# Optimization experiments

Measured on AMD Instinct MI355X. Metric: run time of the kernel, lower is better.

## Reference

```python
import jax, jax.numpy as jnp
import numpy as np

LN_EPS = 1e-5
L2_EPS = 1e-12
SCALE = 1.0 / np.sqrt(768.0)
TOPK = 8


def _ln(x, g, b):
    m = jnp.mean(x, axis=-1, keepdims=True)
    v = jnp.mean(jnp.square(x - m), axis=-1, keepdims=True)
    return (x - m) * jax.lax.rsqrt(v + LN_EPS) * g + b


def _l2norm(x):
    n = jnp.sqrt(jnp.sum(jnp.square(x), axis=-1, keepdims=True))
    return x / jnp.maximum(n, L2_EPS)


def _topk_normalize(scores, k):
    # scores: [B, K]; keep top-k, zero rest, renormalize to sum 1
    vals, idx = jax.lax.top_k(scores, k)
    B = scores.shape[0]
    weights = jnp.zeros_like(scores).at[jnp.arange(B)[:, None], idx].set(vals)
    denom = jnp.maximum(jnp.sum(weights, axis=1, keepdims=True), 1e-8)
    return weights / denom


def setup_inputs() -> dict:
    key = jax.random.key(0)
    ks = jax.random.split(key, 8)
    B, N, D, K, H, C = 32, 4096, 768, 64, 3072, 1000
    inp = {
        "patch_tokens": jax.random.normal(ks[0], (B, N, D), jnp.float32),
        "global_features": jax.random.normal(ks[1], (B, D), jnp.float32),
        "base_logits": jax.random.normal(ks[2], (B, C), jnp.float32),
        "bq": jax.random.normal(ks[3], (K, D), jnp.float32) * 0.02,
        "qn_g": jnp.ones((D,)), "qn_b": jnp.zeros((D,)),
        "tn_g": jnp.ones((D,)), "tn_b": jnp.zeros((D,)),
        "bn_g": jnp.ones((D,)), "bn_b": jnp.zeros((D,)),
        "gn_g": jnp.ones((D,)), "gn_b": jnp.zeros((D,)),
        "rln_g": jnp.ones((D,)), "rln_b": jnp.zeros((D,)),
        "rw1": jax.random.normal(ks[4], (D, H), jnp.float32) / np.sqrt(D),
        "rb1": jnp.zeros((H,)),
        "rw2": jax.random.normal(ks[5], (H, 1), jnp.float32) / np.sqrt(H),
        "rb2": jnp.zeros((1,)),
        "hw1": jax.random.normal(ks[6], (2 * D, H), jnp.float32) / np.sqrt(2 * D),
        "hb1": jnp.zeros((H,)),
        "hw2": jax.random.normal(ks[7], (H, C), jnp.float32) / np.sqrt(H),
        "hb2": jnp.zeros((C,)),
    }
    return inp


def reference(patch_tokens, global_features, base_logits, bq,
              qn_g, qn_b, tn_g, tn_b, bn_g, bn_b, gn_g, gn_b,
              rln_g, rln_b, rw1, rb1, rw2, rb2, hw1, hb1, hw2, hb2):
    # normalized cross-attention: K basis queries vs N tokens
    tokens_key = _l2norm(_ln(patch_tokens, tn_g, tn_b))           # [B,N,D]
    queries = _l2norm(_ln(bq, qn_g, qn_b))                        # [K,D]
    attn_logits = jnp.einsum('kd,bnd->bkn', queries, tokens_key) * SCALE
    attn_weights = jax.nn.softmax(attn_logits, axis=-1)           # [B,K,N]
    basis_states = jnp.einsum('bkn,bnd->bkd', attn_weights, patch_tokens)
    # routing head: LN -> Linear -> GELU -> Linear -> softplus
    r = _ln(basis_states, rln_g, rln_b)
    r = jax.nn.gelu(r @ rw1 + rb1, approximate=False)
    routing_scores = jax.nn.softplus((r @ rw2 + rb2)[..., 0])     # [B,K]
    routing_weights = _topk_normalize(routing_scores, TOPK)
    basis_summary = jnp.einsum('bk,bkd->bd', routing_weights, basis_states)
    basis_summary = _ln(basis_summary, bn_g, bn_b)
    global_summary = _ln(global_features, gn_g, gn_b)
    fused = jnp.concatenate([global_summary, basis_summary], axis=-1)
    h = jax.nn.gelu(fused @ hw1 + hb1, approximate=False)
    residual_logits = h @ hw2 + hb2
    final_logits = base_logits + residual_logits
    # diversity loss over basis queries
    bqn = _l2norm(bq)
    gram = bqn @ bqn.T
    diversity_loss = jnp.mean(jnp.square(gram - jnp.eye(gram.shape[0], dtype=gram.dtype)))
    sparse_loss = jnp.mean(routing_scores)
    return (final_logits, residual_logits, routing_weights, sparse_loss, diversity_loss)
```

## Files before the change

kernel.cpp:

```cpp
#include <hip/hip_runtime.h>
#include <math.h>

#define SCALE 0.036084391824351613f

typedef unsigned short us;
typedef __attribute__((ext_vector_type(8))) short short8;
typedef __attribute__((ext_vector_type(4))) short short4s;
typedef __attribute__((ext_vector_type(4))) float f32x4;
#define MFMA16(a, b, c) __builtin_amdgcn_mfma_f32_16x16x32_bf16(a, b, c, 0, 0, 0)

__device__ __forceinline__ us f2bf(float f) {
  unsigned u = __float_as_uint(f);
  unsigned r = (u + 0x7fffu + ((u >> 16) & 1u)) >> 16;
  return (us)r;
}
__device__ __forceinline__ float bf2f(us u) { return __uint_as_float(((unsigned)u) << 16); }

__device__ __forceinline__ void split8(f32x4 a, f32x4 b, short8& hi, short8& lo) {
  float x[8] = {a[0], a[1], a[2], a[3], b[0], b[1], b[2], b[3]};
#pragma unroll
  for (int i = 0; i < 8; i++) {
    us h = f2bf(x[i]);
    hi[i] = (short)h;
    lo[i] = (short)f2bf(x[i] - bf2f(h));
  }
}

__device__ __forceinline__ float blockReduceSum(float v, float* sh) {
#pragma unroll
  for (int o = 32; o > 0; o >>= 1) v += __shfl_xor(v, o, 64);
  int lane = threadIdx.x & 63, wid = threadIdx.x >> 6;
  __syncthreads();
  if (lane == 0) sh[wid] = v;
  __syncthreads();
  float r = sh[0];
  int nw = blockDim.x >> 6;
  for (int i = 1; i < nw; i++) r += sh[i];
  return r;
}

__device__ __forceinline__ float blockReduceMax(float v, float* sh) {
#pragma unroll
  for (int o = 32; o > 0; o >>= 1) v = fmaxf(v, __shfl_xor(v, o, 64));
  int lane = threadIdx.x & 63, wid = threadIdx.x >> 6;
  __syncthreads();
  if (lane == 0) sh[wid] = v;
  __syncthreads();
  float r = sh[0];
  int nw = blockDim.x >> 6;
  for (int i = 1; i < nw; i++) r = fmaxf(r, sh[i]);
  return r;
}

__device__ __forceinline__ float gelu_exact(float x) {
  return 0.5f * x * (1.0f + erff(x * 0.7071067811865476f));
}

__global__ void __launch_bounds__(256) k_prep_queries(
    const float* __restrict__ bq, const float* __restrict__ qn_g, const float* __restrict__ qn_b,
    const float* __restrict__ tn_g, const float* __restrict__ tn_b,
    us* __restrict__ qgh, us* __restrict__ qgl,
    float* __restrict__ s1, float* __restrict__ qb,
    float* __restrict__ bqn, float* __restrict__ gcons) {
  __shared__ float sh[8];
  int k = blockIdx.x, t = threadIdx.x;
  const float* xr = bq + (size_t)k * 768;
  float x0 = xr[t], x1 = xr[t + 256], x2 = xr[t + 512];
  float sx = blockReduceSum(x0 + x1 + x2, sh);
  float sxx = blockReduceSum(x0 * x0 + x1 * x1 + x2 * x2, sh);
  float mean = sx * (1.0f / 768.0f);
  float var = fmaxf(sxx * (1.0f / 768.0f) - mean * mean, 0.0f);
  float rs = rsqrtf(var + 1e-5f);
  float y0 = (x0 - mean) * rs * qn_g[t] + qn_b[t];
  float y1 = (x1 - mean) * rs * qn_g[t + 256] + qn_b[t + 256];
  float y2 = (x2 - mean) * rs * qn_g[t + 512] + qn_b[t + 512];
  float ss = blockReduceSum(y0 * y0 + y1 * y1 + y2 * y2, sh);
  float inv = 1.0f / fmaxf(sqrtf(ss), 1e-12f);
  float q0 = y0 * inv, q1 = y1 * inv, q2 = y2 * inv;
  float tg0 = tn_g[t], tg1 = tn_g[t + 256], tg2 = tn_g[t + 512];
  float tb0 = tn_b[t], tb1 = tn_b[t + 256], tb2 = tn_b[t + 512];
  float g0 = q0 * tg0, g1 = q1 * tg1, g2 = q2 * tg2;
  us h0 = f2bf(g0), h1 = f2bf(g1), h2 = f2bf(g2);
  qgh[(size_t)k * 768 + t] = h0;
  qgh[(size_t)k * 768 + t + 256] = h1;
  qgh[(size_t)k * 768 + t + 512] = h2;
  qgl[(size_t)k * 768 + t] = f2bf(g0 - bf2f(h0));
  qgl[(size_t)k * 768 + t + 256] = f2bf(g1 - bf2f(h1));
  qgl[(size_t)k * 768 + t + 512] = f2bf(g2 - bf2f(h2));
  float s1p = blockReduceSum(g0 + g1 + g2, sh);
  float qbp = blockReduceSum(q0 * tb0 + q1 * tb1 + q2 * tb2, sh);
  if (t == 0) { s1[k] = s1p; qb[k] = qbp; }
  float inv2 = 1.0f / fmaxf(sqrtf(sxx), 1e-12f);
  bqn[(size_t)k * 768 + t] = x0 * inv2;
  bqn[(size_t)k * 768 + t + 256] = x1 * inv2;
  bqn[(size_t)k * 768 + t + 512] = x2 * inv2;
  float sggp = blockReduceSum(tg0 * tg0 + tg1 * tg1 + tg2 * tg2, sh);
  float sgbp = blockReduceSum(tg0 * tb0 + tg1 * tb1 + tg2 * tb2, sh);
  float sbbp = blockReduceSum(tb0 * tb0 + tb1 * tb1 + tb2 * tb2, sh);
  if (k == 0 && t == 0) { gcons[0] = sggp; gcons[1] = sgbp; gcons[2] = sbbp; }
}

__global__ void __launch_bounds__(256) k_gram(const float* __restrict__ bqn,
                                              float* __restrict__ gpart) {
  __shared__ float bk[768];
  __shared__ float arr[64];
  int k = blockIdx.x, t = threadIdx.x;
  bk[t] = bqn[(size_t)k * 768 + t];
  bk[t + 256] = bqn[(size_t)k * 768 + t + 256];
  bk[t + 512] = bqn[(size_t)k * 768 + t + 512];
  __syncthreads();
  int j = t >> 2, sub = t & 3;
  const float* bj = bqn + (size_t)j * 768 + sub * 192;
  float v = 0.0f;
  for (int d = 0; d < 192; d++) v += bk[sub * 192 + d] * bj[d];
  v += __shfl_xor(v, 1, 64);
  v += __shfl_xor(v, 2, 64);
  if (sub == 0) { float e = v - (j == k ? 1.0f : 0.0f); arr[j] = e * e; }
  __syncthreads();
  if (t < 64) {
    float s = arr[t];
#pragma unroll
    for (int o = 32; o > 0; o >>= 1) s += __shfl_xor(s, o, 64);
    if (t == 0) gpart[k] = s;
  }
}

__global__ void __launch_bounds__(256) k_w1t(const float* __restrict__ rw1,
                                             us* __restrict__ w1th, us* __restrict__ w1tl) {
  __shared__ float tl[32][33];
  int d0 = blockIdx.x * 32, h0 = blockIdx.y * 32;
  int t = threadIdx.x, tx = t & 31, ty = t >> 5;
#pragma unroll
  for (int j = 0; j < 4; j++)
    tl[ty + j * 8][tx] = rw1[(size_t)(d0 + ty + j * 8) * 3072 + h0 + tx];
  __syncthreads();
#pragma unroll
  for (int j = 0; j < 4; j++) {
    float v = tl[tx][ty + j * 8];
    us h = f2bf(v);
    w1th[(size_t)(h0 + ty + j * 8) * 768 + d0 + tx] = h;
    w1tl[(size_t)(h0 + ty + j * 8) * 768 + d0 + tx] = f2bf(v - bf2f(h));
  }
}

__global__ void __launch_bounds__(256) k_attn_mfma(
    const float* __restrict__ x, const us* __restrict__ qgh, const us* __restrict__ qgl,
    const float* __restrict__ s1v, const float* __restrict__ qbv,
    const float* __restrict__ tng, const float* __restrict__ tnb,
    const float* __restrict__ gcons, float* __restrict__ L) {
  __shared__ __align__(16) us qsh[64 * 32], qsl[64 * 32];
  __shared__ __align__(16) us xsh[128 * 32], xsl[128 * 32];
  __shared__ float sA[128], sB[128], sC[128];
  const int b = blockIdx.y, n0 = blockIdx.x * 128;
  const int t = threadIdx.x, w = t >> 6, l = t & 63;
  const int sr = t >> 2, sq = t & 3;
  const us* qsrcH = qgh + (size_t)sr * 768 + sq * 8;
  const us* qsrcL = qgl + (size_t)sr * 768 + sq * 8;
  const float* xsrc = x + ((size_t)b * 4096 + n0 + sr) * 768 + sq * 8;
  f32x4 acc[4][2];
#pragma unroll
  for (int i = 0; i < 4; i++)
#pragma unroll
    for (int j = 0; j < 2; j++) acc[i][j] = (f32x4){0.f, 0.f, 0.f, 0.f};
  float s0x = 0, s0xx = 0, s0a = 0, s0b = 0, s0c = 0;
  float t1x = 0, t1xx = 0, t1a = 0, t1b = 0, t1c = 0;
  short8 qh = *(const short8*)qsrcH, ql = *(const short8*)qsrcL;
  f32x4 x0a = *(const f32x4*)xsrc, x0b = *(const f32x4*)(xsrc + 4);
  f32x4 x1a = *(const f32x4*)(xsrc + (size_t)64 * 768);
  f32x4 x1b = *(const f32x4*)(xsrc + (size_t)64 * 768 + 4);
  for (int dk = 0; dk < 768; dk += 32) {
    f32x4 ga = *(const f32x4*)(tng + dk + sq * 8);
    f32x4 gA = *(const f32x4*)(tng + dk + sq * 8 + 4);
    f32x4 ba = *(const f32x4*)(tnb + dk + sq * 8);
    f32x4 bA = *(const f32x4*)(tnb + dk + sq * 8 + 4);
#pragma unroll
    for (int i = 0; i < 4; i++) {
      float g1 = ga[i], g2 = gA[i], b1 = ba[i], b2 = bA[i];
      float xv = x0a[i]; float gx = g1 * xv;
      s0x += xv; s0xx = fmaf(xv, xv, s0xx);
      s0a = fmaf(gx, gx, s0a); s0b = fmaf(g1, gx, s0b); s0c = fmaf(b1, gx, s0c);
      xv = x0b[i]; gx = g2 * xv;
      s0x += xv; s0xx = fmaf(xv, xv, s0xx);
      s0a = fmaf(gx, gx, s0a); s0b = fmaf(g2, gx, s0b); s0c = fmaf(b2, gx, s0c);
      xv = x1a[i]; gx = g1 * xv;
      t1x += xv; t1xx = fmaf(xv, xv, t1xx);
      t1a = fmaf(gx, gx, t1a); t1b = fmaf(g1, gx, t1b); t1c = fmaf(b1, gx, t1c);
      xv = x1b[i]; gx = g2 * xv;
      t1x += xv; t1xx = fmaf(xv, xv, t1xx);
      t1a = fmaf(gx, gx, t1a); t1b = fmaf(g2, gx, t1b); t1c = fmaf(b2, gx, t1c);
    }
    short8 hi, lo;
    __syncthreads();
    *(short8*)&qsh[sr * 32 + sq * 8] = qh; *(short8*)&qsl[sr * 32 + sq * 8] = ql;
    split8(x0a, x0b, hi, lo);
    *(short8*)&xsh[sr * 32 + sq * 8] = hi; *(short8*)&xsl[sr * 32 + sq * 8] = lo;
    split8(x1a, x1b, hi, lo);
    *(short8*)&xsh[(sr + 64) * 32 + sq * 8] = hi; *(short8*)&xsl[(sr + 64) * 32 + sq * 8] = lo;
    __syncthreads();
    if (dk + 32 < 768) {
      int d2 = dk + 32;
      qh = *(const short8*)(qsrcH + d2); ql = *(const short8*)(qsrcL + d2);
      x0a = *(const f32x4*)(xsrc + d2); x0b = *(const f32x4*)(xsrc + d2 + 4);
      x1a = *(const f32x4*)(xsrc + (size_t)64 * 768 + d2);
      x1b = *(const f32x4*)(xsrc + (size_t)64 * 768 + d2 + 4);
    }
    short8 ah[4], al[4];
#pragma unroll
    for (int kt = 0; kt < 4; kt++) {
      int off = (kt * 16 + (l & 15)) * 32 + (l >> 4) * 8;
      ah[kt] = *(const short8*)&qsh[off];
      al[kt] = *(const short8*)&qsl[off];
    }
#pragma unroll
    for (int nt = 0; nt < 2; nt++) {
      int off = (w * 32 + nt * 16 + (l & 15)) * 32 + (l >> 4) * 8;
      short8 bh = *(const short8*)&xsh[off];
      short8 bl = *(const short8*)&xsl[off];
#pragma unroll
      for (int kt = 0; kt < 4; kt++) {
        acc[kt][nt] = MFMA16(ah[kt], bh, acc[kt][nt]);
        acc[kt][nt] = MFMA16(ah[kt], bl, acc[kt][nt]);
        acc[kt][nt] = MFMA16(al[kt], bh, acc[kt][nt]);
        acc[kt][nt] = MFMA16(al[kt], bl, acc[kt][nt]);
      }
    }
  }
  float sgg = gcons[0], sgb = gcons[1], sbb = gcons[2];
#define R4(v) v += __shfl_xor(v, 1, 64); v += __shfl_xor(v, 2, 64)
  R4(s0x); R4(s0xx); R4(s0a); R4(s0b); R4(s0c);
  R4(t1x); R4(t1xx); R4(t1a); R4(t1b); R4(t1c);
#undef R4
  if (sq == 0) {
    {
      float m = s0x * (1.0f / 768.0f);
      float var = fmaxf(s0xx * (1.0f / 768.0f) - m * m, 0.0f);
      float rs = rsqrtf(var + 1e-5f);
      float ss = fmaxf(rs * rs * (s0a - 2.0f * m * s0b + m * m * sgg) +
                       2.0f * rs * (s0c - m * sgb) + sbb, 0.0f);
      float inv = 1.0f / fmaxf(sqrtf(ss), 1e-12f);
      float A = SCALE * inv * rs;
      sA[sr] = A; sB[sr] = A * m; sC[sr] = SCALE * inv;
    }
    {
      float m = t1x * (1.0f / 768.0f);
      float var = fmaxf(t1xx * (1.0f / 768.0f) - m * m, 0.0f);
      float rs = rsqrtf(var + 1e-5f);
      float ss = fmaxf(rs * rs * (t1a - 2.0f * m * t1b + m * m * sgg) +
                       2.0f * rs * (t1c - m * sgb) + sbb, 0.0f);
      float inv = 1.0f / fmaxf(sqrtf(ss), 1e-12f);
      float A = SCALE * inv * rs;
      sA[sr + 64] = A; sB[sr + 64] = A * m; sC[sr + 64] = SCALE * inv;
    }
  }
  __syncthreads();
#pragma unroll
  for (int nt = 0; nt < 2; nt++) {
    int nn = w * 32 + nt * 16 + (l & 15);
    int n = n0 + nn;
    float Av = sA[nn], Bv = sB[nn], Cv = sC[nn];
#pragma unroll
    for (int kt = 0; kt < 4; kt++) {
#pragma unroll
      for (int r = 0; r < 4; r++) {
        int k = kt * 16 + (l >> 4) * 4 + r;
        L[((size_t)b * 64 + k) * 4096 + n] = Av * acc[kt][nt][r] - Bv * s1v[k] + Cv * qbv[k];
      }
    }
  }
}

__global__ void __launch_bounds__(256) k_softmax(float* __restrict__ L) {
  __shared__ float sh[8];
  size_t row = blockIdx.x;
  f32x4* p = (f32x4*)(L + row * 4096);
  int t = threadIdx.x;
  f32x4 v[4];
  float mx = -INFINITY;
#pragma unroll
  for (int i = 0; i < 4; i++) {
    v[i] = p[t + i * 256];
#pragma unroll
    for (int j = 0; j < 4; j++) mx = fmaxf(mx, v[i][j]);
  }
  mx = blockReduceMax(mx, sh);
  float s = 0.0f;
#pragma unroll
  for (int i = 0; i < 4; i++)
#pragma unroll
    for (int j = 0; j < 4; j++) { v[i][j] = expf(v[i][j] - mx); s += v[i][j]; }
  s = blockReduceSum(s, sh);
  float inv = 1.0f / s;
#pragma unroll
  for (int i = 0; i < 4; i++) {
#pragma unroll
    for (int j = 0; j < 4; j++) v[i][j] *= inv;
    p[t + i * 256] = v[i];
  }
}

__global__ void __launch_bounds__(256) k_zero(float* __restrict__ p) {
  ((f32x4*)p)[blockIdx.x * 256 + threadIdx.x] = (f32x4){0.f, 0.f, 0.f, 0.f};
}

__global__ void __launch_bounds__(256) k_pv_mfma(
    const float* __restrict__ x, const float* __restrict__ W, float* __restrict__ S) {
  __shared__ __align__(16) us wth[64 * 32], wtl[64 * 32];
  __shared__ __align__(16) us xth[8 * 32 * 16], xtl[8 * 32 * 16];
  const int b = blockIdx.y, d0 = blockIdx.x * 128, nb = blockIdx.z * 512;
  const int t = threadIdx.x, w = t >> 6, l = t & 63;
  const float* wsrc = W + ((size_t)b * 64 + (t >> 2)) * 4096 + nb + (t & 3) * 8;
  const int gg = t >> 6, nn = (t >> 1) & 31, hh = t & 1;
  const float* xsrc0 = x + ((size_t)b * 4096 + nb + nn) * 768 + d0 + gg * 16 + hh * 8;
  const float* xsrc1 = xsrc0 + 64;
  f32x4 acc[4][2];
#pragma unroll
  for (int i = 0; i < 4; i++)
#pragma unroll
    for (int j = 0; j < 2; j++) acc[i][j] = (f32x4){0.f, 0.f, 0.f, 0.f};
  f32x4 w0a = *(const f32x4*)wsrc, w0b = *(const f32x4*)(wsrc + 4);
  f32x4 xa0 = *(const f32x4*)xsrc0, xb0 = *(const f32x4*)(xsrc0 + 4);
  f32x4 xa1 = *(const f32x4*)xsrc1, xb1 = *(const f32x4*)(xsrc1 + 4);
  for (int ns = 0; ns < 512; ns += 32) {
    short8 hi, lo;
    __syncthreads();
    split8(w0a, w0b, hi, lo);
    *(short8*)&wth[(t >> 2) * 32 + (t & 3) * 8] = hi;
    *(short8*)&wtl[(t >> 2) * 32 + (t & 3) * 8] = lo;
    split8(xa0, xb0, hi, lo);
    *(short8*)&xth[(size_t)t * 8] = hi; *(short8*)&xtl[(size_t)t * 8] = lo;
    split8(xa1, xb1, hi, lo);
    *(short8*)&xth[((size_t)t + 256) * 8] = hi; *(short8*)&xtl[((size_t)t + 256) * 8] = lo;
    __syncthreads();
    if (ns + 32 < 512) {
      w0a = *(const f32x4*)(wsrc + ns + 32); w0b = *(const f32x4*)(wsrc + ns + 36);
      const float* p0 = xsrc0 + (size_t)(ns + 32) * 768;
      xa0 = *(const f32x4*)p0; xb0 = *(const f32x4*)(p0 + 4);
      xa1 = *(const f32x4*)(p0 + 64); xb1 = *(const f32x4*)(p0 + 68);
    }
    short8 ah[4], al[4];
#pragma unroll
    for (int kt = 0; kt < 4; kt++) {
      int off = (kt * 16 + (l & 15)) * 32 + (l >> 4) * 8;
      ah[kt] = *(const short8*)&wth[off];
      al[kt] = *(const short8*)&wtl[off];
    }
#pragma unroll
    for (int dt = 0; dt < 2; dt++) {
      const us* gph = &xth[(2 * w + dt) * 512];
      const us* gpl = &xtl[(2 * w + dt) * 512];
      int rb = (l >> 4) * 8, cc = l & 15;
      short8 bh, bl;
#pragma unroll
      for (int i = 0; i < 8; i++) {
        bh[i] = (short)gph[(rb + i) * 16 + cc];
        bl[i] = (short)gpl[(rb + i) * 16 + cc];
      }
#pragma unroll
      for (int kt = 0; kt < 4; kt++) {
        acc[kt][dt] = MFMA16(ah[kt], bh, acc[kt][dt]);
        acc[kt][dt] = MFMA16(ah[kt], bl, acc[kt][dt]);
        acc[kt][dt] = MFMA16(al[kt], bh, acc[kt][dt]);
        acc[kt][dt] = MFMA16(al[kt], bl, acc[kt][dt]);
      }
    }
  }
#pragma unroll
  for (int dt = 0; dt < 2; dt++) {
    int d = d0 + w * 32 + dt * 16 + (l & 15);
#pragma unroll
    for (int kt = 0; kt < 4; kt++) {
#pragma unroll
      for (int r = 0; r < 4; r++) {
        int k = kt * 16 + (l >> 4) * 4 + r;
        atomicAdd(&S[((size_t)b * 64 + k) * 768 + d], acc[kt][dt][r]);
      }
    }
  }
}

__global__ void __launch_bounds__(256) k_ln768(
    const float* __restrict__ in, const float* __restrict__ g, const float* __restrict__ b,
    us* __restrict__ outh, us* __restrict__ outl) {
  int wid = threadIdx.x >> 6, lane = threadIdx.x & 63;
  size_t row = (size_t)blockIdx.x * 4 + wid;
  const f32x4* xr = (const f32x4*)(in + row * 768);
  f32x4 v[3];
  float sx = 0, sxx = 0;
#pragma unroll
  for (int j = 0; j < 3; j++) {
    v[j] = xr[lane + j * 64];
#pragma unroll
    for (int i = 0; i < 4; i++) { sx += v[j][i]; sxx = fmaf(v[j][i], v[j][i], sxx); }
  }
#pragma unroll
  for (int o = 32; o > 0; o >>= 1) { sx += __shfl_xor(sx, o, 64); sxx += __shfl_xor(sxx, o, 64); }
  float mean = sx * (1.0f / 768.0f);
  float var = fmaxf(sxx * (1.0f / 768.0f) - mean * mean, 0.0f);
  float rs = rsqrtf(var + 1e-5f);
  const f32x4* gp = (const f32x4*)g;
  const f32x4* bp = (const f32x4*)b;
#pragma unroll
  for (int j = 0; j < 3; j++) {
    f32x4 gv = gp[lane + j * 64], bv = bp[lane + j * 64];
    short4s h4, l4;
#pragma unroll
    for (int i = 0; i < 4; i++) {
      float y = (v[j][i] - mean) * rs * gv[i] + bv[i];
      us h = f2bf(y);
      h4[i] = (short)h;
      l4[i] = (short)f2bf(y - bf2f(h));
    }
    int e = (lane + j * 64) * 4;
    *(short4s*)&outh[row * 768 + e] = h4;
    *(short4s*)&outl[row * 768 + e] = l4;
  }
}

__global__ void __launch_bounds__(256) k_rh_mfma(
    const us* __restrict__ rhh, const us* __restrict__ rhl,
    const us* __restrict__ w1th, const us* __restrict__ w1tl,
    const float* __restrict__ rb1, float* __restrict__ rh) {
  __shared__ __align__(16) us ash[64 * 32], asl[64 * 32];
  __shared__ __align__(16) us bsh[128 * 32], bsl[128 * 32];
  const int h0 = blockIdx.x * 128, m0 = blockIdx.y * 64;
  const int t = threadIdx.x, w = t >> 6, l = t & 63;
  const int sr = t >> 2, sq = t & 3;
  const us* aH = rhh + (size_t)(m0 + sr) * 768 + sq * 8;
  const us* aL = rhl + (size_t)(m0 + sr) * 768 + sq * 8;
  const us* bH = w1th + (size_t)(h0 + sr) * 768 + sq * 8;
  const us* bL = w1tl + (size_t)(h0 + sr) * 768 + sq * 8;
  f32x4 acc[4][2];
#pragma unroll
  for (int i = 0; i < 4; i++)
#pragma unroll
    for (int j = 0; j < 2; j++) acc[i][j] = (f32x4){0.f, 0.f, 0.f, 0.f};
  short8 a0h = *(const short8*)aH, a0l = *(const short8*)aL;
  short8 b0h = *(const short8*)bH, b0l = *(const short8*)bL;
  short8 b1h = *(const short8*)(bH + (size_t)64 * 768);
  short8 b1l = *(const short8*)(bL + (size_t)64 * 768);
  for (int dk = 0; dk < 768; dk += 32) {
    __syncthreads();
    *(short8*)&ash[sr * 32 + sq * 8] = a0h; *(short8*)&asl[sr * 32 + sq * 8] = a0l;
    *(short8*)&bsh[sr * 32 + sq * 8] = b0h; *(short8*)&bsl[sr * 32 + sq * 8] = b0l;
    *(short8*)&bsh[(sr + 64) * 32 + sq * 8] = b1h; *(short8*)&bsl[(sr + 64) * 32 + sq * 8] = b1l;
    __syncthreads();
    if (dk + 32 < 768) {
      int d2 = dk + 32;
      a0h = *(const short8*)(aH + d2); a0l = *(const short8*)(aL + d2);
      b0h = *(const short8*)(bH + d2); b0l = *(const short8*)(bL + d2);
      b1h = *(const short8*)(bH + (size_t)64 * 768 + d2);
      b1l = *(const short8*)(bL + (size_t)64 * 768 + d2);
    }
    short8 ah[4], al[4];
#pragma unroll
    for (int kt = 0; kt < 4; kt++) {
      int off = (kt * 16 + (l & 15)) * 32 + (l >> 4) * 8;
      ah[kt] = *(const short8*)&ash[off];
      al[kt] = *(const short8*)&asl[off];
    }
#pragma unroll
    for (int nt = 0; nt < 2; nt++) {
      int off = (w * 32 + nt * 16 + (l & 15)) * 32 + (l >> 4) * 8;
      short8 bh = *(const short8*)&bsh[off];
      short8 bl = *(const short8*)&bsl[off];
#pragma unroll
      for (int kt = 0; kt < 4; kt++) {
        acc[kt][nt] = MFMA16(ah[kt], bh, acc[kt][nt]);
        acc[kt][nt] = MFMA16(ah[kt], bl, acc[kt][nt]);
        acc[kt][nt] = MFMA16(al[kt], bh, acc[kt][nt]);
        acc[kt][nt] = MFMA16(al[kt], bl, acc[kt][nt]);
      }
    }
  }
#pragma unroll
  for (int nt = 0; nt < 2; nt++) {
    int h = h0 + w * 32 + nt * 16 + (l & 15);
    float bias = rb1[h];
#pragma unroll
    for (int kt = 0; kt < 4; kt++) {
#pragma unroll
      for (int r2 = 0; r2 < 4; r2++) {
        int m = m0 + kt * 16 + (l >> 4) * 4 + r2;
        rh[(size_t)m * 3072 + h] = gelu_exact(acc[kt][nt][r2] + bias);
      }
    }
  }
}

__global__ void __launch_bounds__(256) k_scores(
    const float* __restrict__ rh, const float* __restrict__ rw2, const float* __restrict__ rb2,
    float* __restrict__ scores) {
  __shared__ float sh[8];
  size_t row = blockIdx.x;
  const float* p = rh + row * 3072;
  int t = threadIdx.x;
  float s = 0.0f;
  for (int i = t; i < 3072; i += 256) s = fmaf(p[i], rw2[i], s);
  s = blockReduceSum(s, sh);
  if (t == 0) {
    float z = s + rb2[0];
    scores[row] = fmaxf(z, 0.0f) + log1pf(expf(-fabsf(z)));
  }
}

__global__ void __launch_bounds__(64) k_topk(
    const float* __restrict__ scores, float* __restrict__ rw_ws, float* __restrict__ rw_out) {
  int b = blockIdx.x, lane = threadIdx.x;
  float s = scores[b * 64 + lane];
  bool sel = false;
  for (int it = 0; it < 8; it++) {
    float v = sel ? -INFINITY : s;
    int idx = lane;
#pragma unroll
    for (int o = 32; o > 0; o >>= 1) {
      float v2 = __shfl_xor(v, o, 64);
      int i2 = __shfl_xor(idx, o, 64);
      if (v2 > v || (v2 == v && i2 < idx)) { v = v2; idx = i2; }
    }
    if (lane == idx) sel = true;
  }
  float w = sel ? s : 0.0f;
  float tot = w;
#pragma unroll
  for (int o = 32; o > 0; o >>= 1) tot += __shfl_xor(tot, o, 64);
  float wt = w / fmaxf(tot, 1e-8f);
  rw_ws[b * 64 + lane] = wt;
  rw_out[b * 64 + lane] = wt;
}

__global__ void __launch_bounds__(256) k_fused(
    const float* __restrict__ bs, const float* __restrict__ rw, const float* __restrict__ gf,
    const float* __restrict__ bn_g, const float* __restrict__ bn_b,
    const float* __restrict__ gn_g, const float* __restrict__ gn_b,
    float* __restrict__ fused) {
  __shared__ float sh[8];
  __shared__ float wsh[64];
  int b = blockIdx.x, t = threadIdx.x;
  if (t < 64) wsh[t] = rw[b * 64 + t];
  __syncthreads();
  float v0 = 0, v1 = 0, v2 = 0;
  const float* bsb = bs + (size_t)b * 64 * 768;
  for (int k = 0; k < 64; k++) {
    float w = wsh[k];
    if (w != 0.0f) {
      v0 = fmaf(w, bsb[(size_t)k * 768 + t], v0);
      v1 = fmaf(w, bsb[(size_t)k * 768 + t + 256], v1);
      v2 = fmaf(w, bsb[(size_t)k * 768 + t + 512], v2);
    }
  }
  float sx = blockReduceSum(v0 + v1 + v2, sh);
  float sxx = blockReduceSum(v0 * v0 + v1 * v1 + v2 * v2, sh);
  float mean = sx * (1.0f / 768.0f);
  float var = fmaxf(sxx * (1.0f / 768.0f) - mean * mean, 0.0f);
  float rs = rsqrtf(var + 1e-5f);
  float* fb = fused + (size_t)b * 1536;
  fb[768 + t] = (v0 - mean) * rs * bn_g[t] + bn_b[t];
  fb[768 + t + 256] = (v1 - mean) * rs * bn_g[t + 256] + bn_b[t + 256];
  fb[768 + t + 512] = (v2 - mean) * rs * bn_g[t + 512] + bn_b[t + 512];
  const float* gr = gf + (size_t)b * 768;
  float g0 = gr[t], g1 = gr[t + 256], g2 = gr[t + 512];
  float gsx = blockReduceSum(g0 + g1 + g2, sh);
  float gsxx = blockReduceSum(g0 * g0 + g1 * g1 + g2 * g2, sh);
  float gm = gsx * (1.0f / 768.0f);
  float gv = fmaxf(gsxx * (1.0f / 768.0f) - gm * gm, 0.0f);
  float grs = rsqrtf(gv + 1e-5f);
  fb[t] = (g0 - gm) * grs * gn_g[t] + gn_b[t];
  fb[t + 256] = (g1 - gm) * grs * gn_g[t + 256] + gn_b[t + 256];
  fb[t + 512] = (g2 - gm) * grs * gn_g[t + 512] + gn_b[t + 512];
}

__global__ void __launch_bounds__(256) k_head1(
    const float* __restrict__ fused, const float* __restrict__ hw1, const float* __restrict__ hb1,
    float* __restrict__ h) {
  __shared__ float fl[2][1536];
  __shared__ float part[2][4][64];
  int bp = blockIdx.y * 2, h0 = blockIdx.x * 64, t = threadIdx.x;
  for (int i = t; i < 1536; i += 256) {
    fl[0][i] = fused[(size_t)bp * 1536 + i];
    fl[1][i] = fused[(size_t)(bp + 1) * 1536 + i];
  }
  __syncthreads();
  int c = t & 63, sl = t >> 6;
  int hh = h0 + c;
  int kbase = sl * 384;
  const float* wp = hw1 + (size_t)kbase * 3072 + hh;
  float a0 = 0.f, a1 = 0.f;
#pragma unroll 8
  for (int k = 0; k < 384; k++) {
    float w = wp[(size_t)k * 3072];
    a0 = fmaf(fl[0][kbase + k], w, a0);
    a1 = fmaf(fl[1][kbase + k], w, a1);
  }
  part[0][sl][c] = a0; part[1][sl][c] = a1;
  __syncthreads();
  if (sl == 0) {
    float bias = hb1[hh];
    float s0 = part[0][0][c] + part[0][1][c] + part[0][2][c] + part[0][3][c];
    float s1_ = part[1][0][c] + part[1][1][c] + part[1][2][c] + part[1][3][c];
    h[(size_t)bp * 3072 + hh] = gelu_exact(s0 + bias);
    h[(size_t)(bp + 1) * 3072 + hh] = gelu_exact(s1_ + bias);
  }
}

__global__ void __launch_bounds__(256) k_head2(
    const float* __restrict__ h, const float* __restrict__ hw2, const float* __restrict__ hb2,
    const float* __restrict__ base, float* __restrict__ out) {
  __shared__ float hl[2][3072];
  __shared__ float part[2][4][64];
  int bp = blockIdx.y * 2, c0 = blockIdx.x * 64, t = threadIdx.x;
  for (int i = t; i < 3072; i += 256) {
    hl[0][i] = h[(size_t)bp * 3072 + i];
    hl[1][i] = h[(size_t)(bp + 1) * 3072 + i];
  }
  __syncthreads();
  int c = t & 63, sl = t >> 6;
  int cc = c0 + c;
  int csafe = cc < 1000 ? cc : 999;
  int kbase = sl * 768;
  const float* wp = hw2 + (size_t)kbase * 1000 + csafe;
  float a0 = 0.f, a1 = 0.f;
#pragma unroll 8
  for (int k = 0; k < 768; k++) {
    float w = wp[(size_t)k * 1000];
    a0 = fmaf(hl[0][kbase + k], w, a0);
    a1 = fmaf(hl[1][kbase + k], w, a1);
  }
  part[0][sl][c] = a0; part[1][sl][c] = a1;
  __syncthreads();
  if (sl == 0 && cc < 1000) {
    float bias = hb2[cc];
    float s0 = part[0][0][c] + part[0][1][c] + part[0][2][c] + part[0][3][c] + bias;
    float s1_ = part[1][0][c] + part[1][1][c] + part[1][2][c] + part[1][3][c] + bias;
    out[32000 + bp * 1000 + cc] = s0;
    out[bp * 1000 + cc] = base[bp * 1000 + cc] + s0;
    out[32000 + (bp + 1) * 1000 + cc] = s1_;
    out[(bp + 1) * 1000 + cc] = base[(bp + 1) * 1000 + cc] + s1_;
  }
}

__global__ void __launch_bounds__(256) k_losses(
    const float* __restrict__ scores, const float* __restrict__ gpart, float* __restrict__ out) {
  __shared__ float sh[8];
  int t = threadIdx.x;
  float s = 0.0f;
#pragma unroll
  for (int i = 0; i < 8; i++) s += scores[t + i * 256];
  s = blockReduceSum(s, sh);
  float gsum = (t < 64) ? gpart[t] : 0.0f;
  gsum = blockReduceSum(gsum, sh);
  if (t == 0) {
    out[66048] = s * (1.0f / 2048.0f);
    out[66049] = gsum * (1.0f / 4096.0f);
  }
}

extern "C" void kernel_launch(void* const* d_in, const int* in_sizes, int n_in,
                              void* d_out, int out_size, void* d_ws, size_t ws_size,
                              hipStream_t stream) {
  const float* patch = (const float*)d_in[0];
  const float* gfeat = (const float*)d_in[1];
  const float* base  = (const float*)d_in[2];
  const float* bq    = (const float*)d_in[3];
  const float* qn_g  = (const float*)d_in[4];
  const float* qn_b  = (const float*)d_in[5];
  const float* tn_g  = (const float*)d_in[6];
  const float* tn_b  = (const float*)d_in[7];
  const float* bn_g  = (const float*)d_in[8];
  const float* bn_b  = (const float*)d_in[9];
  const float* gn_g  = (const float*)d_in[10];
  const float* gn_b  = (const float*)d_in[11];
  const float* rln_g = (const float*)d_in[12];
  const float* rln_b = (const float*)d_in[13];
  const float* rw1   = (const float*)d_in[14];
  const float* rb1   = (const float*)d_in[15];
  const float* rw2   = (const float*)d_in[16];
  const float* rb2   = (const float*)d_in[17];
  const float* hw1   = (const float*)d_in[18];
  const float* hb1   = (const float*)d_in[19];
  const float* hw2   = (const float*)d_in[20];
  const float* hb2   = (const float*)d_in[21];
  float* ws = (float*)d_ws;
  float* out = (float*)d_out;

  float* s1     = ws + 0;
  float* qb     = ws + 64;
  float* gcons  = ws + 128;
  float* gpart  = ws + 160;
  float* scores = ws + 256;
  float* rw_ws  = ws + 2304;
  float* fused  = ws + 4352;
  float* hbuf   = ws + 53504;
  float* bqn    = ws + 151808;
  us*    qgh    = (us*)(ws + 200960);
  us*    qgl    = (us*)(ws + 225536);
  us*    w1th   = (us*)(ws + 250112);
  us*    w1tl   = (us*)(ws + 1429760);
  us*    rhh    = (us*)(ws + 2609408);
  us*    rhl    = (us*)(ws + 3395840);
  float* bs     = ws + 4182272;
  float* L      = ws + 5755136;
  float* rh     = L;

  k_prep_queries<<<dim3(64), 256, 0, stream>>>(bq, qn_g, qn_b, tn_g, tn_b,
                                               qgh, qgl, s1, qb, bqn, gcons);
  k_gram<<<dim3(64), 256, 0, stream>>>(bqn, gpart);
  k_w1t<<<dim3(24, 96), 256, 0, stream>>>(rw1, w1th, w1tl);
  k_attn_mfma<<<dim3(32, 32), 256, 0, stream>>>(patch, qgh, qgl, s1, qb, tn_g, tn_b, gcons, L);
  k_softmax<<<dim3(2048), 256, 0, stream>>>(L);
  k_zero<<<dim3(1536), 256, 0, stream>>>(bs);
  k_pv_mfma<<<dim3(6, 32, 8), 256, 0, stream>>>(patch, L, bs);
  k_ln768<<<dim3(512), 256, 0, stream>>>(bs, rln_g, rln_b, rhh, rhl);
  k_rh_mfma<<<dim3(24, 32), 256, 0, stream>>>(rhh, rhl, w1th, w1tl, rb1, rh);
  k_scores<<<dim3(2048), 256, 0, stream>>>(rh, rw2, rb2, scores);
  k_topk<<<dim3(32), 64, 0, stream>>>(scores, rw_ws, out + 64000);
  k_fused<<<dim3(32), 256, 0, stream>>>(bs, rw_ws, gfeat, bn_g, bn_b, gn_g, gn_b, fused);
  k_head1<<<dim3(48, 16), 256, 0, stream>>>(fused, hw1, hb1, hbuf);
  k_head2<<<dim3(16, 16), 256, 0, stream>>>(hbuf, hw2, hb2, base, out);
  k_losses<<<dim3(1), 256, 0, stream>>>(scores, gpart, out);
}
```

Measured before the change: 434.1 us.

## Fuse softmax normalization into PV kernel and scores/topk into neighbors

The softmax kernel now only computes each row's max and inverse sum, and the PV GEMM applies exp and the normalization while loading attention weights. This removes one full write of the 32x64x4096 logits buffer. The second-layer routing projection is folded into the routing MFMA epilogue using shuffle reductions and atomics, so the hidden activations are never stored. Top-k moves into k_fused, and k_zero is widened so it also clears the score accumulator. The cost is redundant exp work in PV: each logit is exponentiated once per d-tile, six times in total. Atomic accumulation also makes the summation order nondeterministic.

```diff
diff --git a/kernel.cpp b/kernel.cpp
--- a/kernel.cpp
+++ b/kernel.cpp
@@ -269,10 +269,12 @@
   }
 }
 
-__global__ void __launch_bounds__(256) k_softmax(float* __restrict__ L) {
+__global__ void __launch_bounds__(256) k_rowstat(const float* __restrict__ L,
+                                                 float* __restrict__ rowm,
+                                                 float* __restrict__ rowinv) {
   __shared__ float sh[8];
   size_t row = blockIdx.x;
-  f32x4* p = (f32x4*)(L + row * 4096);
+  const f32x4* p = (const f32x4*)(L + row * 4096);
   int t = threadIdx.x;
   f32x4 v[4];
   float mx = -INFINITY;
@@ -287,15 +289,9 @@
 #pragma unroll
   for (int i = 0; i < 4; i++)
 #pragma unroll
-    for (int j = 0; j < 4; j++) { v[i][j] = expf(v[i][j] - mx); s += v[i][j]; }
+    for (int j = 0; j < 4; j++) s += expf(v[i][j] - mx);
   s = blockReduceSum(s, sh);
-  float inv = 1.0f / s;
-#pragma unroll
-  for (int i = 0; i < 4; i++) {
-#pragma unroll
-    for (int j = 0; j < 4; j++) v[i][j] *= inv;
-    p[t + i * 256] = v[i];
-  }
+  if (t == 0) { rowm[row] = mx; rowinv[row] = 1.0f / s; }
 }
 
 __global__ void __launch_bounds__(256) k_zero(float* __restrict__ p) {
@@ -303,12 +299,17 @@
 }
 
 __global__ void __launch_bounds__(256) k_pv_mfma(
-    const float* __restrict__ x, const float* __restrict__ W, float* __restrict__ S) {
+    const float* __restrict__ x, const float* __restrict__ W,
+    const float* __restrict__ rowm, const float* __restrict__ rowinv,
+    float* __restrict__ S) {
   __shared__ __align__(16) us wth[64 * 32], wtl[64 * 32];
   __shared__ __align__(16) us xth[8 * 32 * 16], xtl[8 * 32 * 16];
   const int b = blockIdx.y, d0 = blockIdx.x * 128, nb = blockIdx.z * 512;
   const int t = threadIdx.x, w = t >> 6, l = t & 63;
-  const float* wsrc = W + ((size_t)b * 64 + (t >> 2)) * 4096 + nb + (t & 3) * 8;
+  const int krow = t >> 2;
+  const float* wsrc = W + ((size_t)b * 64 + krow) * 4096 + nb + (t & 3) * 8;
+  const float mr = rowm[b * 64 + krow];
+  const float ir = rowinv[b * 64 + krow];
   const int gg = t >> 6, nn = (t >> 1) & 31, hh = t & 1;
   const float* xsrc0 = x + ((size_t)b * 4096 + nb + nn) * 768 + d0 + gg * 16 + hh * 8;
   const float* xsrc1 = xsrc0 + 64;
@@ -322,10 +323,16 @@
   f32x4 xa1 = *(const f32x4*)xsrc1, xb1 = *(const f32x4*)(xsrc1 + 4);
   for (int ns = 0; ns < 512; ns += 32) {
     short8 hi, lo;
+    f32x4 e0, e1;
+#pragma unroll
+    for (int i = 0; i < 4; i++) {
+      e0[i] = expf(w0a[i] - mr) * ir;
+      e1[i] = expf(w0b[i] - mr) * ir;
+    }
     __syncthreads();
-    split8(w0a, w0b, hi, lo);
-    *(short8*)&wth[(t >> 2) * 32 + (t & 3) * 8] = hi;
-    *(short8*)&wtl[(t >> 2) * 32 + (t & 3) * 8] = lo;
+    split8(e0, e1, hi, lo);
+    *(short8*)&wth[krow * 32 + (t & 3) * 8] = hi;
+    *(short8*)&wtl[krow * 32 + (t & 3) * 8] = lo;
     split8(xa0, xb0, hi, lo);
     *(short8*)&xth[(size_t)t * 8] = hi; *(short8*)&xtl[(size_t)t * 8] = lo;
     split8(xa1, xb1, hi, lo);
@@ -419,9 +426,11 @@
 __global__ void __launch_bounds__(256) k_rh_mfma(
     const us* __restrict__ rhh, const us* __restrict__ rhl,
     const us* __restrict__ w1th, const us* __restrict__ w1tl,
-    const float* __restrict__ rb1, float* __restrict__ rh) {
+    const float* __restrict__ rb1, const float* __restrict__ rw2,
+    float* __restrict__ scores_raw) {
   __shared__ __align__(16) us ash[64 * 32], asl[64 * 32];
   __shared__ __align__(16) us bsh[128 * 32], bsl[128 * 32];
+  __shared__ float spart[4][64];
   const int h0 = blockIdx.x * 128, m0 = blockIdx.y * 64;
   const int t = threadIdx.x, w = t >> 6, l = t & 63;
   const int sr = t >> 2, sq = t & 3;
@@ -472,71 +481,80 @@
       }
     }
   }
+  float psum[4][4];
+#pragma unroll
+  for (int kt = 0; kt < 4; kt++)
+#pragma unroll
+    for (int r = 0; r < 4; r++) psum[kt][r] = 0.f;
 #pragma unroll
   for (int nt = 0; nt < 2; nt++) {
     int h = h0 + w * 32 + nt * 16 + (l & 15);
     float bias = rb1[h];
+    float rw2v = rw2[h];
 #pragma unroll
     for (int kt = 0; kt < 4; kt++) {
 #pragma unroll
-      for (int r2 = 0; r2 < 4; r2++) {
-        int m = m0 + kt * 16 + (l >> 4) * 4 + r2;
-        rh[(size_t)m * 3072 + h] = gelu_exact(acc[kt][nt][r2] + bias);
+      for (int r = 0; r < 4; r++) {
+        float g = gelu_exact(acc[kt][nt][r] + bias);
+        psum[kt][r] = fmaf(g, rw2v, psum[kt][r]);
       }
     }
   }
-}
-
-__global__ void __launch_bounds__(256) k_scores(
-    const float* __restrict__ rh, const float* __restrict__ rw2, const float* __restrict__ rb2,
-    float* __restrict__ scores) {
-  __shared__ float sh[8];
-  size_t row = blockIdx.x;
-  const float* p = rh + row * 3072;
-  int t = threadIdx.x;
-  float s = 0.0f;
-  for (int i = t; i < 3072; i += 256) s = fmaf(p[i], rw2[i], s);
-  s = blockReduceSum(s, sh);
-  if (t == 0) {
-    float z = s + rb2[0];
-    scores[row] = fmaxf(z, 0.0f) + log1pf(expf(-fabsf(z)));
-  }
-}
-
-__global__ void __launch_bounds__(64) k_topk(
-    const float* __restrict__ scores, float* __restrict__ rw_ws, float* __restrict__ rw_out) {
-  int b = blockIdx.x, lane = threadIdx.x;
-  float s = scores[b * 64 + lane];
-  bool sel = false;
-  for (int it = 0; it < 8; it++) {
-    float v = sel ? -INFINITY : s;
-    int idx = lane;
-#pragma unroll
-    for (int o = 32; o > 0; o >>= 1) {
-      float v2 = __shfl_xor(v, o, 64);
-      int i2 = __shfl_xor(idx, o, 64);
-      if (v2 > v || (v2 == v && i2 < idx)) { v = v2; idx = i2; }
-    }
-    if (lane == idx) sel = true;
-  }
-  float w = sel ? s : 0.0f;
-  float tot = w;
-#pragma unroll
-  for (int o = 32; o > 0; o >>= 1) tot += __shfl_xor(tot, o, 64);
-  float wt = w / fmaxf(tot, 1e-8f);
-  rw_ws[b * 64 + lane] = wt;
-  rw_out[b * 64 + lane] = wt;
+#pragma unroll
+  for (int kt = 0; kt < 4; kt++)
+#pragma unroll
+    for (int r = 0; r < 4; r++) {
+      float v = psum[kt][r];
+      v += __shfl_xor(v, 1, 64);
+      v += __shfl_xor(v, 2, 64);
+      v += __shfl_xor(v, 4, 64);
+      v += __shfl_xor(v, 8, 64);
+      psum[kt][r] = v;
+    }
+  if ((l & 15) == 0) {
+#pragma unroll
+    for (int kt = 0; kt < 4; kt++)
+#pragma unroll
+      for (int r = 0; r < 4; r++)
+        spart[w][kt * 16 + (l >> 4) * 4 + r] = psum[kt][r];
+  }
+  __syncthreads();
+  if (t < 64)
+    atomicAdd(&scores_raw[m0 + t], spart[0][t] + spart[1][t] + spart[2][t] + spart[3][t]);
 }
 
 __global__ void __launch_bounds__(256) k_fused(
-    const float* __restrict__ bs, const float* __restrict__ rw, const float* __restrict__ gf,
+    const float* __restrict__ bs, const float* __restrict__ scores_raw,
+    const float* __restrict__ rb2, const float* __restrict__ gf,
     const float* __restrict__ bn_g, const float* __restrict__ bn_b,
     const float* __restrict__ gn_g, const float* __restrict__ gn_b,
-    float* __restrict__ fused) {
+    float* __restrict__ fused, float* __restrict__ rw_out) {
   __shared__ float sh[8];
   __shared__ float wsh[64];
   int b = blockIdx.x, t = threadIdx.x;
-  if (t < 64) wsh[t] = rw[b * 64 + t];
+  if (t < 64) {
+    float z = scores_raw[b * 64 + t] + rb2[0];
+    float s = fmaxf(z, 0.0f) + log1pf(expf(-fabsf(z)));
+    bool sel = false;
+    for (int it = 0; it < 8; it++) {
+      float v = sel ? -INFINITY : s;
+      int idx = t;
+#pragma unroll
+      for (int o = 32; o > 0; o >>= 1) {
+        float v2 = __shfl_xor(v, o, 64);
+        int i2 = __shfl_xor(idx, o, 64);
+        if (v2 > v || (v2 == v && i2 < idx)) { v = v2; idx = i2; }
+      }
+      if (t == idx) sel = true;
+    }
+    float wv = sel ? s : 0.0f;
+    float tot = wv;
+#pragma unroll
+    for (int o = 32; o > 0; o >>= 1) tot += __shfl_xor(tot, o, 64);
+    float wt = wv / fmaxf(tot, 1e-8f);
+    wsh[t] = wt;
+    rw_out[b * 64 + t] = wt;
+  }
   __syncthreads();
   float v0 = 0, v1 = 0, v2 = 0;
   const float* bsb = bs + (size_t)b * 64 * 768;
@@ -639,12 +657,16 @@
 }
 
 __global__ void __launch_bounds__(256) k_losses(
-    const float* __restrict__ scores, const float* __restrict__ gpart, float* __restrict__ out) {
+    const float* __restrict__ scores_raw, const float* __restrict__ rb2,
+    const float* __restrict__ gpart, float* __restrict__ out) {
   __shared__ float sh[8];
   int t = threadIdx.x;
   float s = 0.0f;
 #pragma unroll
-  for (int i = 0; i < 8; i++) s += scores[t + i * 256];
+  for (int i = 0; i < 8; i++) {
+    float z = scores_raw[t + i * 256] + rb2[0];
+    s += fmaxf(z, 0.0f) + log1pf(expf(-fabsf(z)));
+  }
   s = blockReduceSum(s, sh);
   float gsum = (t < 64) ? gpart[t] : 0.0f;
   gsum = blockReduceSum(gsum, sh);
@@ -682,39 +704,38 @@
   float* ws = (float*)d_ws;
   float* out = (float*)d_out;
 
-  float* s1     = ws + 0;
-  float* qb     = ws + 64;
-  float* gcons  = ws + 128;
-  float* gpart  = ws + 160;
-  float* scores = ws + 256;
-  float* rw_ws  = ws + 2304;
-  float* fused  = ws + 4352;
-  float* hbuf   = ws + 53504;
-  float* bqn    = ws + 151808;
-  us*    qgh    = (us*)(ws + 200960);
-  us*    qgl    = (us*)(ws + 225536);
-  us*    w1th   = (us*)(ws + 250112);
-  us*    w1tl   = (us*)(ws + 1429760);
-  us*    rhh    = (us*)(ws + 2609408);
-  us*    rhl    = (us*)(ws + 3395840);
-  float* bs     = ws + 4182272;
-  float* L      = ws + 5755136;
-  float* rh     = L;
+  float* s1      = ws + 0;
+  float* qb      = ws + 64;
+  float* gcons   = ws + 128;
+  float* gpart   = ws + 160;
+  float* rowm    = ws + 224;
+  float* rowinv  = ws + 2272;
+  float* fusedb  = ws + 4320;
+  float* hbuf    = ws + 53472;
+  float* bqn     = ws + 151776;
+  us*    qgh     = (us*)(ws + 200928);
+  us*    qgl     = (us*)(ws + 225504);
+  us*    w1th    = (us*)(ws + 250080);
+  us*    w1tl    = (us*)(ws + 1429728);
+  us*    rhh     = (us*)(ws + 2609376);
+  us*    rhl     = (us*)(ws + 3395808);
+  float* bs      = ws + 4182240;
+  float* scores  = ws + 5755104;
+  float* L       = ws + 5757152;
 
   k_prep_queries<<<dim3(64), 256, 0, stream>>>(bq, qn_g, qn_b, tn_g, tn_b,
                                                qgh, qgl, s1, qb, bqn, gcons);
   k_gram<<<dim3(64), 256, 0, stream>>>(bqn, gpart);
   k_w1t<<<dim3(24, 96), 256, 0, stream>>>(rw1, w1th, w1tl);
   k_attn_mfma<<<dim3(32, 32), 256, 0, stream>>>(patch, qgh, qgl, s1, qb, tn_g, tn_b, gcons, L);
-  k_softmax<<<dim3(2048), 256, 0, stream>>>(L);
-  k_zero<<<dim3(1536), 256, 0, stream>>>(bs);
-  k_pv_mfma<<<dim3(6, 32, 8), 256, 0, stream>>>(patch, L, bs);
+  k_rowstat<<<dim3(2048), 256, 0, stream>>>(L, rowm, rowinv);
+  k_zero<<<dim3(1538), 256, 0, stream>>>(bs);
+  k_pv_mfma<<<dim3(6, 32, 8), 256, 0, stream>>>(patch, L, rowm, rowinv, bs);
   k_ln768<<<dim3(512), 256, 0, stream>>>(bs, rln_g, rln_b, rhh, rhl);
-  k_rh_mfma<<<dim3(24, 32), 256, 0, stream>>>(rhh, rhl, w1th, w1tl, rb1, rh);
-  k_scores<<<dim3(2048), 256, 0, stream>>>(rh, rw2, rb2, scores);
-  k_topk<<<dim3(32), 64, 0, stream>>>(scores, rw_ws, out + 64000);
-  k_fused<<<dim3(32), 256, 0, stream>>>(bs, rw_ws, gfeat, bn_g, bn_b, gn_g, gn_b, fused);
-  k_head1<<<dim3(48, 16), 256, 0, stream>>>(fused, hw1, hb1, hbuf);
+  k_rh_mfma<<<dim3(24, 32), 256, 0, stream>>>(rhh, rhl, w1th, w1tl, rb1, rw2, scores);
+  k_fused<<<dim3(32), 256, 0, stream>>>(bs, scores, rb2, gfeat, bn_g, bn_b, gn_g, gn_b,
+                                        fusedb, out + 64000);
+  k_head1<<<dim3(48, 16), 256, 0, stream>>>(fusedb, hw1, hb1, hbuf);
   k_head2<<<dim3(16, 16), 256, 0, stream>>>(hbuf, hw2, hb2, base, out);
-  k_losses<<<dim3(1), 256, 0, stream>>>(scores, gpart, out);
-}
+  k_losses<<<dim3(1), 256, 0, stream>>>(scores, rb2, gpart, out);
+}
```

Result: faster. 422.5 us (-2.7%).
